# Kernel tuning notes

Measured on AMD Instinct MI355X. Metric: run time of the kernel, lower is better.

Reference implementation:

```python
import jax, jax.numpy as jnp
import numpy as np

MUL = 32          # multiplicity of 0e and 1o channels
NRAD = 8          # radial basis size
NPATH = 7         # TP instructions

# Orthonormal symmetric-traceless basis for the real l=2 irrep -> Cartesian map
_B = np.zeros((5, 3, 3))
_s2 = 1.0 / np.sqrt(2.0)
_B[0, 0, 1] = _B[0, 1, 0] = _s2                      # xy
_B[1, 1, 2] = _B[1, 2, 1] = _s2                      # yz
_B[2] = np.diag([-1.0, -1.0, 2.0]) / np.sqrt(6.0)    # 2z^2-x^2-y^2
_B[3, 0, 2] = _B[3, 2, 0] = _s2                      # xz
_B[4] = np.diag([1.0, -1.0, 0.0]) / np.sqrt(2.0)     # x^2-y^2
# w3j(1,2,1)[i,M,k], Frobenius-normalized to 1 (e3nn convention)
C121 = jnp.asarray(np.transpose(_B, (1, 0, 2)) / np.sqrt(5.0), jnp.float32)
INV_SQRT3 = float(1.0 / np.sqrt(3.0))   # w3j(1,1,0) / w3j(0,1,1) / w3j(1,0,1)
A0 = float(1.0 / np.sqrt(64.0))         # path weight, l=0 outs: sqrt(1/fan_in), fan_in=2*32
A1 = float(np.sqrt(3.0 / 96.0))         # path weight, l=1 out: sqrt((2l+1)/fan_in), fan_in=3*32


def setup_inputs() -> dict:
    key = jax.random.key(0)
    ks = jax.random.split(key, 9)
    N, E = 4096, 32768
    x = jax.random.normal(ks[0], (N, 4 * MUL), jnp.float32)
    edge_attr = jax.random.normal(ks[1], (E, 9), jnp.float32)
    edge_length = jax.random.uniform(ks[2], (E,), jnp.float32) * 5.0
    edge_src = jax.random.randint(ks[3], (E,), 0, N)
    edge_dst = jax.random.randint(ks[4], (E,), 0, N)
    W_fc1 = jax.random.normal(ks[5], (NRAD, 64), jnp.float32)
    W_fc2 = jax.random.normal(ks[6], (64, NPATH * MUL * MUL), jnp.float32)
    W_sc_s = jax.random.normal(ks[7], (MUL, MUL), jnp.float32)
    W_sc_v = jax.random.normal(ks[8], (MUL, MUL), jnp.float32)
    return dict(x=x, edge_attr=edge_attr, edge_length=edge_length,
                edge_src=edge_src, edge_dst=edge_dst,
                W_fc1=W_fc1, W_fc2=W_fc2, W_sc_s=W_sc_s, W_sc_v=W_sc_v)


def reference(x, edge_attr, edge_length, edge_src, edge_dst, W_fc1, W_fc2, W_sc_s, W_sc_v):
    N = x.shape[0]
    # radial Gaussian basis: centers linspace(0,5,8), sigma = spacing
    centers = jnp.linspace(0.0, 5.0, NRAD)
    sigma = 5.0 / (NRAD - 1)
    d = edge_length[:, None] - centers[None, :]
    radial = jnp.exp(-d * d / (2.0 * sigma * sigma))
    # radial MLP -> per-edge TP weights (e3nn FullyConnectedNet: W/sqrt(fan_in), silu)
    h = jax.nn.silu(radial @ (W_fc1 / jnp.sqrt(jnp.float32(NRAD))))
    w = h @ (W_fc2 / jnp.sqrt(jnp.float32(64)))          # [E, 7168]
    W = w.reshape(-1, NPATH, MUL, MUL)                    # [E,7,u,w]
    # split node features: 32x0e scalars + 32x1o vectors
    s = x[:, :MUL]
    v = x[:, MUL:].reshape(N, MUL, 3)
    sj = s[edge_src]                                      # [E,u]
    vj = v[edge_src]                                      # [E,u,3]
    y0 = edge_attr[:, 0]
    y1 = edge_attr[:, 1:4]
    y2 = edge_attr[:, 4:9]
    # tensor-product paths
    t00 = sj * y0[:, None]                                            # 0e x 0e
    t11 = jnp.einsum('eui,ei->eu', vj, y1) * INV_SQRT3                # 1o x 1o -> 0e
    out_s = (jnp.einsum('eu,euw->ew', t00, W[:, 0]) +
             jnp.einsum('eu,euw->ew', t11, W[:, 1])) * A0             # scalars
    out_g = (jnp.einsum('eu,euw->ew', t00, W[:, 2]) +
             jnp.einsum('eu,euw->ew', t11, W[:, 3])) * A0             # gates
    t01 = sj[:, :, None] * y1[:, None, :] * INV_SQRT3                 # 0e x 1o -> 1o
    t10 = vj * (y0[:, None, None] * INV_SQRT3)                        # 1o x 0e -> 1o
    t12 = jnp.einsum('eui,imk,em->euk', vj, C121, y2)                 # 1o x 2e -> 1o
    out_v = (jnp.einsum('euk,euw->ewk', t01, W[:, 4]) +
             jnp.einsum('euk,euw->ewk', t10, W[:, 5]) +
             jnp.einsum('euk,euw->ewk', t12, W[:, 6])) * A1           # [E,w,3]
    m_ij = jnp.concatenate([out_s, out_g, out_v.reshape(-1, 3 * MUL)], axis=1)  # [E,160]
    # scatter-mean over destination nodes
    sums = jax.ops.segment_sum(m_ij, edge_dst, num_segments=N)
    cnt = jax.ops.segment_sum(jnp.ones((m_ij.shape[0],), m_ij.dtype), edge_dst, num_segments=N)
    m_i = sums / jnp.clip(cnt, 1.0)[:, None]
    # gate: silu on scalars, sigmoid gates multiply the 1o block per-channel
    gs = jax.nn.silu(m_i[:, :MUL])
    gate = jax.nn.sigmoid(m_i[:, MUL:2 * MUL])
    gv = m_i[:, 2 * MUL:].reshape(N, MUL, 3) * gate[:, :, None]
    # residual self-connection (e3nn o3.Linear: per-irrep, / sqrt(mul_in))
    inv_sqrt_mul = 1.0 / jnp.sqrt(jnp.float32(MUL))
    h_s = gs + (s @ W_sc_s) * inv_sqrt_mul
    h_v = gv + jnp.einsum('nui,uw->nwi', v, W_sc_v) * inv_sqrt_mul
    # o3.Norm: per-irrep L2 norm over the (2l+1) components
    norm_s = jnp.sqrt(h_s * h_s + 1e-12)
    norm_v = jnp.sqrt(jnp.sum(h_v * h_v, axis=-1) + 1e-12)
    return jnp.concatenate([norm_s, norm_v], axis=1)       # [N, 64]
```

## Files before the change

kernel.cpp:

```cpp
#include <hip/hip_runtime.h>

#define NIVL  256
#define KINV  51.2f
#define KSTEP 0.01953125f
#define TPW   7168
#define BCAP  256
#define DCAP  64
#define NROW  11
#define TSTR  40

typedef __attribute__((ext_vector_type(8))) __bf16 bf16x8;
typedef __attribute__((ext_vector_type(4))) float f32x4;
union FragU { uint4 u; bf16x8 v; };

__device__ __forceinline__ float sigmoidf_(float v) { return 1.f / (1.f + expf(-v)); }
__device__ __forceinline__ unsigned bf16r_(float x) { return (__float_as_uint(x) + 0x8000u) >> 16; }
__device__ __forceinline__ unsigned pk_(float lo, float hi) { return (bf16r_(hi) << 16) | bf16r_(lo); }

__device__ __forceinline__ f32x4 mfma_(bf16x8 a, bf16x8 b, f32x4 c) {
    return __builtin_amdgcn_mfma_f32_16x16x32_bf16(a, b, c, 0, 0, 0);
}

__global__ __launch_bounds__(256)
void prep_kernel(const float* __restrict__ W1, const float* __restrict__ W2,
                 const float* __restrict__ elen, const int* __restrict__ edst,
                 float* __restrict__ T, int* __restrict__ cntL, int* __restrict__ cntD,
                 int* __restrict__ sortedL, int* __restrict__ sortedD, int E)
{
    const int tid = threadIdx.x;
    if (blockIdx.x < 231) {
        __shared__ float hk_s[8][64];
        const int bx = blockIdx.x % 7;
        const int k0 = (blockIdx.x / 7) * 8;
        const int pw = bx * 1024 + tid * 4;
#pragma unroll
        for (int q = 0; q < 2; ++q) {
            int idx = tid + q * 256;
            int kk = idx >> 6, c = idx & 63;
            float L = (float)(k0 + kk) * KSTEP;
            float d = 0.f;
#pragma unroll
            for (int r = 0; r < 8; ++r) {
                float dd = L - (float)r * (5.f / 7.f);
                d += expf(-dd * dd * 0.98f) * W1[r * 64 + c];
            }
            d *= 0.3535533906f;
            hk_s[kk][c] = d * sigmoidf_(d) * 0.125f;
        }
        __syncthreads();
        float4 acc[8];
#pragma unroll
        for (int q = 0; q < 8; ++q) acc[q] = make_float4(0.f, 0.f, 0.f, 0.f);
#pragma unroll 4
        for (int c = 0; c < 64; ++c) {
            float4 w4 = *(const float4*)(W2 + (size_t)c * TPW + pw);
#pragma unroll
            for (int q = 0; q < 8; ++q) {
                float hv = hk_s[q][c];
                acc[q].x = fmaf(hv, w4.x, acc[q].x);
                acc[q].y = fmaf(hv, w4.y, acc[q].y);
                acc[q].z = fmaf(hv, w4.z, acc[q].z);
                acc[q].w = fmaf(hv, w4.w, acc[q].w);
            }
        }
#pragma unroll
        for (int q = 0; q < 8; ++q) {
            int k = k0 + q;
            if (k < 257)
                *(float4*)(T + (size_t)k * TPW + pw) = acc[q];
        }
    } else {
        int e = (blockIdx.x - 231) * 256 + tid;
        if (e < E) {
            float t = elen[e] * KINV;
            int j = (int)t; j = j > 255 ? 255 : j;
            int pos = atomicAdd(&cntL[j], 1);
            if (pos < BCAP) sortedL[j * BCAP + pos] = e;
            int d = edst[e];
            int pd = atomicAdd(&cntD[d], 1);
            if (pd < DCAP) sortedD[d * DCAP + pd] = e;
        }
    }
}

__global__ __launch_bounds__(256, 2)
void fold_kernel(const float* __restrict__ x, const float* __restrict__ ea,
                 const float* __restrict__ elen, const int* __restrict__ esrc,
                 const int* __restrict__ cntL, const int* __restrict__ sortedL,
                 const float* __restrict__ T, float* __restrict__ msg)
{
    const int j = blockIdx.x >> 1, half = blockIdx.x & 1;
    __shared__ uint4 BF[7 * 2 * 2 * 64];
    __shared__ __align__(16) unsigned short TB[2 * NROW * 16 * TSTR];
    __shared__ float ECF[32];
    __shared__ int   ECE[32];
    const int tid = threadIdx.x;

    const float* Trow  = T + (size_t)j * TPW;
    const float* Trow2 = Trow + TPW;
    for (int i = tid; i < 896; i += 256) {
        int pl = i >> 7, rem = i & 127;
        int whs = rem >> 6, lane_s = rem & 63;
        int u0 = (lane_s >> 4) * 8, w = whs * 16 + (lane_s & 15);
        int basei = pl * 1024 + w;
        unsigned ta[4], dd[4];
#pragma unroll
        for (int q = 0; q < 4; ++q) {
            float a0 = Trow[basei + (u0 + 2 * q) * 32];
            float a1 = Trow[basei + (u0 + 2 * q + 1) * 32];
            float b0 = Trow2[basei + (u0 + 2 * q) * 32];
            float b1 = Trow2[basei + (u0 + 2 * q + 1) * 32];
            ta[q] = pk_(a0, a1);
            dd[q] = pk_(b0 - a0, b1 - a1);
        }
        BF[(pl * 4 + whs) * 64 + lane_s]     = make_uint4(ta[0], ta[1], ta[2], ta[3]);
        BF[(pl * 4 + 2 + whs) * 64 + lane_s] = make_uint4(dd[0], dd[1], dd[2], dd[3]);
    }

    const int cnt = min(cntL[j], BCAP);
    const int nchunk = (cnt + 31) >> 5;
    const int wv = tid >> 6, lane = tid & 63;
    const int sg = wv >> 1, wh = wv & 1;
    const int col = lane & 15, quad = lane >> 4;
    const int te = tid & 31, sub = tid >> 5;
    const float I3 = 0.5773502692f, I5 = 0.4472135955f, S2 = 0.7071067812f;
    const float I6 = 0.4082482905f, T6 = 0.8164965809f;
    const float A0 = 0.125f, A1 = 0.1767766953f;

    for (int ci = half; ci < nchunk; ci += 2) {
        const int base = ci << 5;
        const int cntE = min(32, cnt - base);
        __syncthreads();

        {
            const int u0 = sub * 4;
            const int esg = te >> 4, e16 = te & 15;
            float rv[NROW][4];
            if (te < cntE) {
                int e = sortedL[j * BCAP + base + te];
                int src = esrc[e];
                const float* y = ea + (size_t)e * 9;
                float y0 = y[0];
                float y0i  = y0 * I3;
                float y1i0 = y[1] * I3, y1i1 = y[2] * I3, y1i2 = y[3] * I3;
                float a = y[4], b = y[5], c = y[6], d2 = y[7], ee = y[8];
                float M0 = (-c * I6 + ee * S2) * I5;
                float M1 = a * S2 * I5;
                float M2 = d2 * S2 * I5;
                float M3 = a * S2 * I5;
                float M4 = (-c * I6 - ee * S2) * I5;
                float M5 = b * S2 * I5;
                float M6 = d2 * S2 * I5;
                float M7 = b * S2 * I5;
                float M8 = c * T6 * I5;
                if (sub == 0) {
                    float t = elen[e] * KINV;
                    int jj = (int)t; jj = jj > 255 ? 255 : jj;
                    ECF[te] = t - (float)jj;
                    ECE[te] = e;
                }
                const float* xp = x + (size_t)src * 128;
                float s4[4], vv[12];
                *(float4*)s4 = *(const float4*)(xp + u0);
                *(float4*)(vv)     = *(const float4*)(xp + 32 + 3 * u0);
                *(float4*)(vv + 4) = *(const float4*)(xp + 32 + 3 * u0 + 4);
                *(float4*)(vv + 8) = *(const float4*)(xp + 32 + 3 * u0 + 8);
#pragma unroll
                for (int up = 0; up < 4; ++up) {
                    float s = s4[up];
                    float v0 = vv[3 * up], v1 = vv[3 * up + 1], v2 = vv[3 * up + 2];
                    rv[0][up] = s * y0;
                    rv[1][up] = v0 * y1i0 + v1 * y1i1 + v2 * y1i2;
                    rv[2][up] = s * y1i0;
                    rv[3][up] = s * y1i1;
                    rv[4][up] = s * y1i2;
                    rv[5][up] = v0 * y0i;
                    rv[6][up] = v1 * y0i;
                    rv[7][up] = v2 * y0i;
                    rv[8][up]  = v0 * M0 + v1 * M3 + v2 * M6;
                    rv[9][up]  = v0 * M1 + v1 * M4 + v2 * M7;
                    rv[10][up] = v0 * M2 + v1 * M5 + v2 * M8;
                }
            } else {
#pragma unroll
                for (int r = 0; r < NROW; ++r)
#pragma unroll
                    for (int up = 0; up < 4; ++up) rv[r][up] = 0.f;
            }
#pragma unroll
            for (int r = 0; r < NROW; ++r) {
                unsigned lo = pk_(rv[r][0], rv[r][1]);
                unsigned hi = pk_(rv[r][2], rv[r][3]);
                *(uint2*)&TB[((esg * NROW + r) * 16 + e16) * TSTR + u0] = make_uint2(lo, hi);
            }
        }
        __syncthreads();

        f32x4 cS0 = {0,0,0,0}, cS1 = {0,0,0,0}, cG0 = {0,0,0,0}, cG1 = {0,0,0,0};
        f32x4 cV[3][2];
#pragma unroll
        for (int k = 0; k < 3; ++k) { cV[k][0] = (f32x4){0,0,0,0}; cV[k][1] = (f32x4){0,0,0,0}; }

        #define LOADA(r) ({ FragU fa_; fa_.u = *(const uint4*)&TB[((sg * NROW + (r)) * 16 + col) * TSTR + quad * 8]; fa_.v; })
        #define LOADB(p, tad) ({ FragU fb_; fb_.u = BF[((p) * 4 + (tad) * 2 + wh) * 64 + lane]; fb_.v; })

        bf16x8 a0 = LOADA(0), a1 = LOADA(1);
        cS0 = mfma_(a0, LOADB(0, 0), cS0); cS0 = mfma_(a1, LOADB(1, 0), cS0);
        cS1 = mfma_(a0, LOADB(0, 1), cS1); cS1 = mfma_(a1, LOADB(1, 1), cS1);
        cG0 = mfma_(a0, LOADB(2, 0), cG0); cG0 = mfma_(a1, LOADB(3, 0), cG0);
        cG1 = mfma_(a0, LOADB(2, 1), cG1); cG1 = mfma_(a1, LOADB(3, 1), cG1);
#pragma unroll
        for (int k = 0; k < 3; ++k) {
            bf16x8 ak;
            ak = LOADA(2 + k);
            cV[k][0] = mfma_(ak, LOADB(4, 0), cV[k][0]);
            cV[k][1] = mfma_(ak, LOADB(4, 1), cV[k][1]);
            ak = LOADA(5 + k);
            cV[k][0] = mfma_(ak, LOADB(5, 0), cV[k][0]);
            cV[k][1] = mfma_(ak, LOADB(5, 1), cV[k][1]);
            ak = LOADA(8 + k);
            cV[k][0] = mfma_(ak, LOADB(6, 0), cV[k][0]);
            cV[k][1] = mfma_(ak, LOADB(6, 1), cV[k][1]);
        }

        const int w = wh * 16 + col;
#pragma unroll
        for (int reg = 0; reg < 4; ++reg) {
            int e = sg * 16 + quad * 4 + reg;
            if (e < cntE) {
                float f = ECF[e];
                int eid = ECE[e];
                float* mp = msg + (size_t)eid * 160;
                mp[w]            = (cS0[reg] + f * cS1[reg]) * A0;
                mp[32 + w]       = (cG0[reg] + f * cG1[reg]) * A0;
                mp[64 + 3 * w]     = (cV[0][0][reg] + f * cV[0][1][reg]) * A1;
                mp[64 + 3 * w + 1] = (cV[1][0][reg] + f * cV[1][1][reg]) * A1;
                mp[64 + 3 * w + 2] = (cV[2][0][reg] + f * cV[2][1][reg]) * A1;
            }
        }
        #undef LOADA
        #undef LOADB
    }
}

__global__ __launch_bounds__(256)
void node_kernel(const float* __restrict__ x, const float* __restrict__ Wss,
                 const float* __restrict__ Wsv, const float* __restrict__ msg,
                 const int* __restrict__ sortedD, const int* __restrict__ cntD,
                 float* __restrict__ out, int N)
{
    __shared__ float ms[8][160];
    const int tid = threadIdx.x;
    const int n0 = blockIdx.x * 8;
    const float IM = 0.1767766953f;

#pragma unroll
    for (int it = 0; it < 5; ++it) {
        int task = tid + it * 256;
        int nl = task / 160;
        int c = task - nl * 160;
        int n = n0 + nl;
        if (n < N) {
            int cd = cntD[n];
            int cc = cd < DCAP ? cd : DCAP;
            const int* sp = sortedD + n * DCAP;
            float s = 0.f;
            for (int i0 = 0; i0 < cc; i0 += 8) {
                int4 ia = *(const int4*)(sp + i0);
                int4 ib = *(const int4*)(sp + i0 + 4);
                int id[8] = { ia.x, ia.y, ia.z, ia.w, ib.x, ib.y, ib.z, ib.w };
                float p[8];
#pragma unroll
                for (int k = 0; k < 8; ++k)
                    p[k] = (i0 + k < cc) ? msg[(size_t)id[k] * 160 + c] : 0.f;
#pragma unroll
                for (int k = 0; k < 8; ++k) s += p[k];
            }
            ms[nl][c] = s / fmaxf((float)cd, 1.f);
        }
    }
    __syncthreads();

#pragma unroll
    for (int it = 0; it < 2; ++it) {
        int task = tid + it * 256;
        int nl = task >> 6, col = task & 63;
        int n = n0 + nl;
        if (n >= N) continue;
        const float* m  = ms[nl];
        const float* xp = x + (size_t)n * 128;
        if (col < 32) {
            int w = col;
            float mval = m[w];
            float gs = mval * sigmoidf_(mval);
            float dot = 0.f;
#pragma unroll 4
            for (int u = 0; u < 32; ++u) dot += xp[u] * Wss[u * 32 + w];
            float hs = gs + dot * IM;
            out[(size_t)n * 64 + w] = sqrtf(hs * hs + 1e-12f);
        } else {
            int w = col - 32;
            float gate = sigmoidf_(m[32 + w]);
            float g0 = m[64 + 3 * w + 0] * gate;
            float g1 = m[64 + 3 * w + 1] * gate;
            float g2 = m[64 + 3 * w + 2] * gate;
            float d0 = 0.f, d1 = 0.f, d2 = 0.f;
#pragma unroll 4
            for (int u = 0; u < 32; ++u) {
                float wv = Wsv[u * 32 + w];
                d0 += xp[32 + 3 * u + 0] * wv;
                d1 += xp[32 + 3 * u + 1] * wv;
                d2 += xp[32 + 3 * u + 2] * wv;
            }
            float h0 = g0 + d0 * IM, h1 = g1 + d1 * IM, h2 = g2 + d2 * IM;
            out[(size_t)n * 64 + 32 + w] = sqrtf(h0 * h0 + h1 * h1 + h2 * h2 + 1e-12f);
        }
    }
}

extern "C" void kernel_launch(void* const* d_in, const int* in_sizes, int n_in,
                              void* d_out, int out_size, void* d_ws, size_t ws_size,
                              hipStream_t stream)
{
    const float* x    = (const float*)d_in[0];
    const float* ea   = (const float*)d_in[1];
    const float* elen = (const float*)d_in[2];
    const int*   esrc = (const int*)d_in[3];
    const int*   edst = (const int*)d_in[4];
    const float* W1   = (const float*)d_in[5];
    const float* W2   = (const float*)d_in[6];
    const float* Wss  = (const float*)d_in[7];
    const float* Wsv  = (const float*)d_in[8];
    float* out = (float*)d_out;

    const int N = in_sizes[0] / 128;
    const int E = in_sizes[2];

    float* T      = (float*)d_ws;
    float* msg    = T + (size_t)257 * TPW;
    int*   cntL   = (int*)(msg + (size_t)E * 160);
    int*   cntD   = cntL + 256;
    int*   sortedL= cntD + N;
    int*   sortedD= sortedL + 256 * BCAP;

    hipMemsetAsync(cntL, 0, (size_t)(256 + N) * sizeof(int), stream);

    prep_kernel<<<231 + (E + 255) / 256, 256, 0, stream>>>(W1, W2, elen, edst, T, cntL, cntD, sortedL, sortedD, E);
    fold_kernel<<<NIVL * 2, 256, 0, stream>>>(x, ea, elen, esrc, cntL, sortedL, T, msg);
    node_kernel<<<(N + 7) / 8, 256, 0, stream>>>(x, Wss, Wsv, msg, sortedD, cntD, out, N);
}
```

Before: 144.7 us.

## Precompute packed per-edge records in prep and prefetch them in fold kernel

The binning phase of prep now writes a 64-byte packed record per edge (fraction, src, edge id, scaled spherical-harmonic terms and the six unique symmetric coupling coefficients) instead of just the edge index. The fold kernel reads these records, prefetching the next chunk's record into registers across iterations and issuing the x gather before the barrier. This removes the dependent index-then-attribute gather chain from fold. The prep T-table tiling also drops from 8 to 4 rows per block (455 blocks) for more parallelism. In exchange, prep does more work and global writes, and fold uses more registers.

Result: faster. 138.6 us (-4.2%).

```diff
diff --git a/kernel.cpp b/kernel.cpp
--- a/kernel.cpp
+++ b/kernel.cpp
@@ -8,6 +8,7 @@
 #define DCAP  64
 #define NROW  11
 #define TSTR  40
+#define PREPT 455
 
 typedef __attribute__((ext_vector_type(8))) __bf16 bf16x8;
 typedef __attribute__((ext_vector_type(4))) float f32x4;
@@ -23,20 +24,19 @@
 
 __global__ __launch_bounds__(256)
 void prep_kernel(const float* __restrict__ W1, const float* __restrict__ W2,
-                 const float* __restrict__ elen, const int* __restrict__ edst,
+                 const float* __restrict__ elen, const int* __restrict__ esrc,
+                 const int* __restrict__ edst, const float* __restrict__ ea,
                  float* __restrict__ T, int* __restrict__ cntL, int* __restrict__ cntD,
-                 int* __restrict__ sortedL, int* __restrict__ sortedD, int E)
+                 float* __restrict__ erec, int* __restrict__ sortedD, int E)
 {
     const int tid = threadIdx.x;
-    if (blockIdx.x < 231) {
-        __shared__ float hk_s[8][64];
+    if (blockIdx.x < PREPT) {
+        __shared__ float hk_s[4][64];
         const int bx = blockIdx.x % 7;
-        const int k0 = (blockIdx.x / 7) * 8;
+        const int k0 = (blockIdx.x / 7) * 4;
         const int pw = bx * 1024 + tid * 4;
-#pragma unroll
-        for (int q = 0; q < 2; ++q) {
-            int idx = tid + q * 256;
-            int kk = idx >> 6, c = idx & 63;
+        {
+            int kk = tid >> 6, c = tid & 63;
             float L = (float)(k0 + kk) * KSTEP;
             float d = 0.f;
 #pragma unroll
@@ -48,14 +48,14 @@
             hk_s[kk][c] = d * sigmoidf_(d) * 0.125f;
         }
         __syncthreads();
-        float4 acc[8];
-#pragma unroll
-        for (int q = 0; q < 8; ++q) acc[q] = make_float4(0.f, 0.f, 0.f, 0.f);
+        float4 acc[4];
+#pragma unroll
+        for (int q = 0; q < 4; ++q) acc[q] = make_float4(0.f, 0.f, 0.f, 0.f);
 #pragma unroll 4
         for (int c = 0; c < 64; ++c) {
             float4 w4 = *(const float4*)(W2 + (size_t)c * TPW + pw);
 #pragma unroll
-            for (int q = 0; q < 8; ++q) {
+            for (int q = 0; q < 4; ++q) {
                 float hv = hk_s[q][c];
                 acc[q].x = fmaf(hv, w4.x, acc[q].x);
                 acc[q].y = fmaf(hv, w4.y, acc[q].y);
@@ -64,18 +64,40 @@
             }
         }
 #pragma unroll
-        for (int q = 0; q < 8; ++q) {
+        for (int q = 0; q < 4; ++q) {
             int k = k0 + q;
             if (k < 257)
                 *(float4*)(T + (size_t)k * TPW + pw) = acc[q];
         }
     } else {
-        int e = (blockIdx.x - 231) * 256 + tid;
+        const float I3 = 0.5773502692f, I5 = 0.4472135955f, S2 = 0.7071067812f;
+        const float I6 = 0.4082482905f, T6 = 0.8164965809f;
+        int e = (blockIdx.x - PREPT) * 256 + tid;
         if (e < E) {
             float t = elen[e] * KINV;
             int j = (int)t; j = j > 255 ? 255 : j;
             int pos = atomicAdd(&cntL[j], 1);
-            if (pos < BCAP) sortedL[j * BCAP + pos] = e;
+            if (pos < BCAP) {
+                const float* y = ea + (size_t)e * 9;
+                float y0 = y[0];
+                float a = y[4], b = y[5], c = y[6], d2 = y[7], ee = y[8];
+                float4 r0, r1, r2, r3;
+                r0.x = t - (float)j;
+                r0.y = __int_as_float(esrc[e]);
+                r0.z = __int_as_float(e);
+                r0.w = y0;
+                r1.x = y0 * I3;
+                r1.y = y[1] * I3; r1.z = y[2] * I3; r1.w = y[3] * I3;
+                r2.x = (-c * I6 + ee * S2) * I5;
+                r2.y = a * S2 * I5;
+                r2.z = d2 * S2 * I5;
+                r2.w = (-c * I6 - ee * S2) * I5;
+                r3.x = b * S2 * I5;
+                r3.y = c * T6 * I5;
+                r3.z = 0.f; r3.w = 0.f;
+                float4* dst = (float4*)(erec + ((size_t)j * BCAP + pos) * 16);
+                dst[0] = r0; dst[1] = r1; dst[2] = r2; dst[3] = r3;
+            }
             int d = edst[e];
             int pd = atomicAdd(&cntD[d], 1);
             if (pd < DCAP) sortedD[d * DCAP + pd] = e;
@@ -84,10 +106,9 @@
 }
 
 __global__ __launch_bounds__(256, 2)
-void fold_kernel(const float* __restrict__ x, const float* __restrict__ ea,
-                 const float* __restrict__ elen, const int* __restrict__ esrc,
-                 const int* __restrict__ cntL, const int* __restrict__ sortedL,
-                 const float* __restrict__ T, float* __restrict__ msg)
+void fold_kernel(const float* __restrict__ x, const int* __restrict__ cntL,
+                 const float* __restrict__ erec, const float* __restrict__ T,
+                 float* __restrict__ msg)
 {
     const int j = blockIdx.x >> 1, half = blockIdx.x & 1;
     __shared__ uint4 BF[7 * 2 * 2 * 64];
@@ -95,6 +116,19 @@
     __shared__ float ECF[32];
     __shared__ int   ECE[32];
     const int tid = threadIdx.x;
+
+    const int cnt = min(cntL[j], BCAP);
+    const int nchunk = (cnt + 31) >> 5;
+    const int te = tid & 31, sub = tid >> 5;
+
+    float4 er0 = {0,0,0,0}, er1 = {0,0,0,0}, er2 = {0,0,0,0}, er3 = {0,0,0,0};
+    if (half < nchunk) {
+        int ce = min(32, cnt - (half << 5));
+        if (te < ce) {
+            const float4* rp = (const float4*)(erec + ((size_t)j * BCAP + (half << 5) + te) * 16);
+            er0 = rp[0]; er1 = rp[1]; er2 = rp[2]; er3 = rp[3];
+        }
+    }
 
     const float* Trow  = T + (size_t)j * TPW;
     const float* Trow2 = Trow + TPW;
@@ -117,54 +151,49 @@
         BF[(pl * 4 + 2 + whs) * 64 + lane_s] = make_uint4(dd[0], dd[1], dd[2], dd[3]);
     }
 
-    const int cnt = min(cntL[j], BCAP);
-    const int nchunk = (cnt + 31) >> 5;
     const int wv = tid >> 6, lane = tid & 63;
     const int sg = wv >> 1, wh = wv & 1;
     const int col = lane & 15, quad = lane >> 4;
-    const int te = tid & 31, sub = tid >> 5;
-    const float I3 = 0.5773502692f, I5 = 0.4472135955f, S2 = 0.7071067812f;
-    const float I6 = 0.4082482905f, T6 = 0.8164965809f;
     const float A0 = 0.125f, A1 = 0.1767766953f;
 
     for (int ci = half; ci < nchunk; ci += 2) {
         const int base = ci << 5;
         const int cntE = min(32, cnt - base);
+
+        const int u0 = sub * 4;
+        float s4[4], vv[12];
+        if (te < cntE) {
+            int src = __float_as_int(er0.y);
+            const float* xp = x + (size_t)src * 128;
+            *(float4*)s4 = *(const float4*)(xp + u0);
+            *(float4*)(vv)     = *(const float4*)(xp + 32 + 3 * u0);
+            *(float4*)(vv + 4) = *(const float4*)(xp + 32 + 3 * u0 + 4);
+            *(float4*)(vv + 8) = *(const float4*)(xp + 32 + 3 * u0 + 8);
+        }
+        float4 nr0 = {0,0,0,0}, nr1 = {0,0,0,0}, nr2 = {0,0,0,0}, nr3 = {0,0,0,0};
+        const int cin = ci + 2;
+        if (cin < nchunk) {
+            int ce2 = min(32, cnt - (cin << 5));
+            if (te < ce2) {
+                const float4* rp = (const float4*)(erec + ((size_t)j * BCAP + (cin << 5) + te) * 16);
+                nr0 = rp[0]; nr1 = rp[1]; nr2 = rp[2]; nr3 = rp[3];
+            }
+        }
+
         __syncthreads();
 
         {
-            const int u0 = sub * 4;
             const int esg = te >> 4, e16 = te & 15;
             float rv[NROW][4];
             if (te < cntE) {
-                int e = sortedL[j * BCAP + base + te];
-                int src = esrc[e];
-                const float* y = ea + (size_t)e * 9;
-                float y0 = y[0];
-                float y0i  = y0 * I3;
-                float y1i0 = y[1] * I3, y1i1 = y[2] * I3, y1i2 = y[3] * I3;
-                float a = y[4], b = y[5], c = y[6], d2 = y[7], ee = y[8];
-                float M0 = (-c * I6 + ee * S2) * I5;
-                float M1 = a * S2 * I5;
-                float M2 = d2 * S2 * I5;
-                float M3 = a * S2 * I5;
-                float M4 = (-c * I6 - ee * S2) * I5;
-                float M5 = b * S2 * I5;
-                float M6 = d2 * S2 * I5;
-                float M7 = b * S2 * I5;
-                float M8 = c * T6 * I5;
+                float y0 = er0.w;
+                float y0i = er1.x, y1i0 = er1.y, y1i1 = er1.z, y1i2 = er1.w;
+                float M0 = er2.x, M1 = er2.y, M2 = er2.z, M4 = er2.w;
+                float M5 = er3.x, M8 = er3.y;
                 if (sub == 0) {
-                    float t = elen[e] * KINV;
-                    int jj = (int)t; jj = jj > 255 ? 255 : jj;
-                    ECF[te] = t - (float)jj;
-                    ECE[te] = e;
+                    ECF[te] = er0.x;
+                    ECE[te] = __float_as_int(er0.z);
                 }
-                const float* xp = x + (size_t)src * 128;
-                float s4[4], vv[12];
-                *(float4*)s4 = *(const float4*)(xp + u0);
-                *(float4*)(vv)     = *(const float4*)(xp + 32 + 3 * u0);
-                *(float4*)(vv + 4) = *(const float4*)(xp + 32 + 3 * u0 + 4);
-                *(float4*)(vv + 8) = *(const float4*)(xp + 32 + 3 * u0 + 8);
 #pragma unroll
                 for (int up = 0; up < 4; ++up) {
                     float s = s4[up];
@@ -177,8 +206,8 @@
                     rv[5][up] = v0 * y0i;
                     rv[6][up] = v1 * y0i;
                     rv[7][up] = v2 * y0i;
-                    rv[8][up]  = v0 * M0 + v1 * M3 + v2 * M6;
-                    rv[9][up]  = v0 * M1 + v1 * M4 + v2 * M7;
+                    rv[8][up]  = v0 * M0 + v1 * M1 + v2 * M2;
+                    rv[9][up]  = v0 * M1 + v1 * M4 + v2 * M5;
                     rv[10][up] = v0 * M2 + v1 * M5 + v2 * M8;
                 }
             } else {
@@ -240,6 +269,7 @@
         }
         #undef LOADA
         #undef LOADB
+        er0 = nr0; er1 = nr1; er2 = nr2; er3 = nr3;
     }
 }
 
@@ -338,14 +368,14 @@
 
     float* T      = (float*)d_ws;
     float* msg    = T + (size_t)257 * TPW;
-    int*   cntL   = (int*)(msg + (size_t)E * 160);
+    float* erec   = msg + (size_t)E * 160;
+    int*   cntL   = (int*)(erec + (size_t)256 * BCAP * 16);
     int*   cntD   = cntL + 256;
-    int*   sortedL= cntD + N;
-    int*   sortedD= sortedL + 256 * BCAP;
+    int*   sortedD= cntD + N;
 
     hipMemsetAsync(cntL, 0, (size_t)(256 + N) * sizeof(int), stream);
 
-    prep_kernel<<<231 + (E + 255) / 256, 256, 0, stream>>>(W1, W2, elen, edst, T, cntL, cntD, sortedL, sortedD, E);
-    fold_kernel<<<NIVL * 2, 256, 0, stream>>>(x, ea, elen, esrc, cntL, sortedL, T, msg);
+    prep_kernel<<<PREPT + (E + 255) / 256, 256, 0, stream>>>(W1, W2, elen, esrc, edst, ea, T, cntL, cntD, erec, sortedD, E);
+    fold_kernel<<<NIVL * 2, 256, 0, stream>>>(x, cntL, erec, T, msg);
     node_kernel<<<(N + 7) / 8, 256, 0, stream>>>(x, Wss, Wsv, msg, sortedD, cntD, out, N);
 }
```
